# Kernel optimization log

Measured on AMD Instinct MI355X. Metric: run time of the kernel, lower is better.

Reference implementation:

```python
import jax, jax.numpy as jnp
import numpy as np

NEG_SLOPE = 0.01  # nn.LeakyReLU default

def _leaky(x):
    return jnp.where(x >= 0, x, NEG_SLOPE * x)

def setup_inputs() -> dict:
    key = jax.random.key(0)
    ks = jax.random.split(key, 8)
    in_ch = 64
    B, H, W = 8, 256, 256
    x = jax.random.normal(ks[0], (B, 2 * in_ch, H, W), dtype=jnp.float32)
    dims = [(64, 128), (32, 64), (16, 32), (8, 16), (4, 8), (2, 4), (1, 2)]
    inp = {"x": x}
    for i, (o, c) in enumerate(dims):
        # kaiming_normal_ fan_out, relu: std = sqrt(2 / fan_out), fan_out = o*1*1
        std = np.sqrt(2.0 / o).astype(np.float32)
        inp[f"w{i+1}"] = jax.random.normal(ks[i + 1], (o, c), dtype=jnp.float32) * std
    return inp

def reference(x, w1, w2, w3, w4, w5, w6, w7):
    # Each 1x1 conv (bias-free) is a per-pixel matmul over channels.
    h = x
    for w in (w1, w2, w3, w4, w5, w6):
        h = _leaky(jnp.einsum('bchw,oc->bohw', h, w))
    out = jnp.einsum('bchw,oc->bohw', h, w7)  # final conv, no activation
    return out
```

## Files before the change

kernel.cpp:

```cpp
#include <hip/hip_runtime.h>


#define NEG_SLOPE 0.01f

typedef __attribute__((ext_vector_type(8))) short bf16x8;
typedef __attribute__((ext_vector_type(4))) float f32x4;

__device__ __forceinline__ float leaky(float v) { return v >= 0.f ? v : NEG_SLOPE * v; }

__device__ __forceinline__ short f2b(float f) {
    unsigned u = __float_as_uint(f);
    u += 0x7fffu + ((u >> 16) & 1u);
    return (short)(u >> 16);
}

__device__ __forceinline__ unsigned pk(float a, float b) {
    return (unsigned)(unsigned short)f2b(a) | ((unsigned)(unsigned short)f2b(b) << 16);
}

__device__ __forceinline__ bf16x8 loadA(const float* __restrict__ wsrc, int C, int m, int k) {
    const float* pr = wsrc + m * C + k;
    f32x4 lo = *(const f32x4*)pr;
    f32x4 hi = *(const f32x4*)(pr + 4);
    bf16x8 r;
    r[0] = f2b(lo[0]); r[1] = f2b(lo[1]); r[2] = f2b(lo[2]); r[3] = f2b(lo[3]);
    r[4] = f2b(hi[0]); r[5] = f2b(hi[1]); r[6] = f2b(hi[2]); r[7] = f2b(hi[3]);
    return r;
}

__global__ __launch_bounds__(256) void fused_mfma_kernel(
    const float* __restrict__ x,
    const float* __restrict__ w1, const float* __restrict__ w2,
    const float* __restrict__ w3, const float* __restrict__ w4,
    const float* __restrict__ w5, const float* __restrict__ w6,
    const float* __restrict__ w7, float* __restrict__ out) {
    constexpr int HW = 65536;

    __shared__ short lds_h1[4][16 * 72];
    __shared__ short lds_h2[4][16 * 40];
    __shared__ float lds_h3[4][64 * 17];
    __shared__ float lds_tw[176];

    const int tid = threadIdx.x;
    if (tid < 128)      lds_tw[tid] = w4[tid];
    else if (tid < 160) lds_tw[tid] = w5[tid - 128];
    else if (tid < 168) lds_tw[tid] = w6[tid - 160];
    else if (tid < 170) lds_tw[tid] = w7[tid - 168];
    __syncthreads();

    const int w    = tid >> 6;
    const int lane = tid & 63;
    const int p    = lane & 15;
    const int q    = lane >> 4;

    const int px0   = blockIdx.x * 256 + w * 64;
    const int batch = px0 >> 16;
    const int pin   = px0 & (HW - 1);
    const float* xb = x + (size_t)batch * 128 * HW;

    bf16x8 a1[4][4];
#pragma unroll
    for (int Mt = 0; Mt < 4; ++Mt)
#pragma unroll
        for (int Ks = 0; Ks < 4; ++Ks)
            a1[Mt][Ks] = loadA(w1, 128, Mt * 16 + p, Ks * 32 + q * 8);
    bf16x8 a2[2][2];
#pragma unroll
    for (int Mt = 0; Mt < 2; ++Mt)
#pragma unroll
        for (int Ks = 0; Ks < 2; ++Ks)
            a2[Mt][Ks] = loadA(w2, 64, Mt * 16 + p, Ks * 32 + q * 8);
    bf16x8 a3 = loadA(w3, 32, p, q * 8);

#pragma unroll
    for (int Nt = 0; Nt < 4; ++Nt) {
        const float* xp = xb + pin + Nt * 16 + p;

        bf16x8 bx[4];
#pragma unroll
        for (int Ks = 0; Ks < 4; ++Ks) {
            float t[8];
#pragma unroll
            for (int j = 0; j < 8; ++j)
                t[j] = xp[(size_t)(Ks * 32 + q * 8 + j) * HW];
#pragma unroll
            for (int j = 0; j < 8; ++j) bx[Ks][j] = f2b(t[j]);
        }

        f32x4 d1[4];
#pragma unroll
        for (int Mt = 0; Mt < 4; ++Mt) {
            f32x4 acc = {0.f, 0.f, 0.f, 0.f};
#pragma unroll
            for (int Ks = 0; Ks < 4; ++Ks)
                acc = __builtin_amdgcn_mfma_f32_16x16x32_bf16(a1[Mt][Ks], bx[Ks], acc, 0, 0, 0);
            d1[Mt] = acc;
        }

        {
            short* h1w = &lds_h1[w][p * 72];
#pragma unroll
            for (int Mt = 0; Mt < 4; ++Mt) {
                uint2 v;
                v.x = pk(leaky(d1[Mt][0]), leaky(d1[Mt][1]));
                v.y = pk(leaky(d1[Mt][2]), leaky(d1[Mt][3]));
                *(uint2*)(h1w + Mt * 16 + q * 4) = v;
            }
        }

        bf16x8 b2[2];
#pragma unroll
        for (int Ks = 0; Ks < 2; ++Ks)
            b2[Ks] = *(const bf16x8*)&lds_h1[w][p * 72 + Ks * 32 + q * 8];

        f32x4 d2[2];
#pragma unroll
        for (int Mt = 0; Mt < 2; ++Mt) {
            f32x4 acc = {0.f, 0.f, 0.f, 0.f};
#pragma unroll
            for (int Ks = 0; Ks < 2; ++Ks)
                acc = __builtin_amdgcn_mfma_f32_16x16x32_bf16(a2[Mt][Ks], b2[Ks], acc, 0, 0, 0);
            d2[Mt] = acc;
        }

        {
            short* h2w = &lds_h2[w][p * 40];
#pragma unroll
            for (int Mt = 0; Mt < 2; ++Mt) {
                uint2 v;
                v.x = pk(leaky(d2[Mt][0]), leaky(d2[Mt][1]));
                v.y = pk(leaky(d2[Mt][2]), leaky(d2[Mt][3]));
                *(uint2*)(h2w + Mt * 16 + q * 4) = v;
            }
        }

        bf16x8 b3 = *(const bf16x8*)&lds_h2[w][p * 40 + q * 8];
        f32x4 zero = {0.f, 0.f, 0.f, 0.f};
        f32x4 d3 = __builtin_amdgcn_mfma_f32_16x16x32_bf16(a3, b3, zero, 0, 0, 0);

        {
            float* h3w = &lds_h3[w][(Nt * 16 + p) * 17 + q * 4];
            h3w[0] = leaky(d3[0]);
            h3w[1] = leaky(d3[1]);
            h3w[2] = leaky(d3[2]);
            h3w[3] = leaky(d3[3]);
        }
    }

    const float* h3r = &lds_h3[w][lane * 17];
    float h[16];
#pragma unroll
    for (int c = 0; c < 16; ++c) h[c] = h3r[c];

    float g4[8];
#pragma unroll
    for (int o = 0; o < 8; ++o) {
        float a = 0.f;
#pragma unroll
        for (int c = 0; c < 16; ++c) a = fmaf(lds_tw[o * 16 + c], h[c], a);
        g4[o] = leaky(a);
    }
    float g5[4];
#pragma unroll
    for (int o = 0; o < 4; ++o) {
        float a = 0.f;
#pragma unroll
        for (int c = 0; c < 8; ++c) a = fmaf(lds_tw[128 + o * 8 + c], g4[c], a);
        g5[o] = leaky(a);
    }
    float g6[2];
#pragma unroll
    for (int o = 0; o < 2; ++o) {
        float a = 0.f;
#pragma unroll
        for (int c = 0; c < 4; ++c) a = fmaf(lds_tw[160 + o * 4 + c], g5[c], a);
        g6[o] = leaky(a);
    }
    out[px0 + lane] = fmaf(lds_tw[168], g6[0], lds_tw[169] * g6[1]);
}

extern "C" void kernel_launch(void* const* d_in, const int* in_sizes, int n_in,
                              void* d_out, int out_size, void* d_ws, size_t ws_size,
                              hipStream_t stream) {
    const float* x  = (const float*)d_in[0];
    const float* w1 = (const float*)d_in[1];
    const float* w2 = (const float*)d_in[2];
    const float* w3 = (const float*)d_in[3];
    const float* w4 = (const float*)d_in[4];
    const float* w5 = (const float*)d_in[5];
    const float* w6 = (const float*)d_in[6];
    const float* w7 = (const float*)d_in[7];
    float* out = (float*)d_out;

    const int P = 8 * 256 * 256;
    fused_mfma_kernel<<<P / 256, 256, 0, stream>>>(x, w1, w2, w3, w4, w5, w6, w7, out);
}
```

Measured before the change: 439.7 us.

## Stage input channels through double-buffered LDS with async global-to-LDS copies

The kernel now loads x with 16-byte-per-lane async global_load_lds copies into a double-buffered LDS tile of 32 channels by 128 pixels. The first-layer MFMA loop iterates over K-chunks with the next chunk prefetched, replacing the old narrow, poorly coalesced per-lane scalar loads strided by HW. Blocks now cover 128 pixels (32 per wave, two N-tiles), and the intermediate LDS buffers are unioned into one per-wave scratch area. Occupancy is hinted via launch_bounds(256,2). The trade-off is extra block barriers per K-chunk and only half the lanes active in the scalar tail layers.

```diff
diff --git a/kernel.cpp b/kernel.cpp
--- a/kernel.cpp
+++ b/kernel.cpp
@@ -2,9 +2,11 @@
 
 
 #define NEG_SLOPE 0.01f
+constexpr int HW = 65536;
 
 typedef __attribute__((ext_vector_type(8))) short bf16x8;
 typedef __attribute__((ext_vector_type(4))) float f32x4;
+typedef __attribute__((ext_vector_type(2))) float f32x2;
 
 __device__ __forceinline__ float leaky(float v) { return v >= 0.f ? v : NEG_SLOPE * v; }
 
@@ -13,32 +15,33 @@
     u += 0x7fffu + ((u >> 16) & 1u);
     return (short)(u >> 16);
 }
-
-__device__ __forceinline__ unsigned pk(float a, float b) {
+__device__ __forceinline__ unsigned pk2(float a, float b) {
     return (unsigned)(unsigned short)f2b(a) | ((unsigned)(unsigned short)f2b(b) << 16);
 }
 
 __device__ __forceinline__ bf16x8 loadA(const float* __restrict__ wsrc, int C, int m, int k) {
-    const float* pr = wsrc + m * C + k;
-    f32x4 lo = *(const f32x4*)pr;
-    f32x4 hi = *(const f32x4*)(pr + 4);
-    bf16x8 r;
-    r[0] = f2b(lo[0]); r[1] = f2b(lo[1]); r[2] = f2b(lo[2]); r[3] = f2b(lo[3]);
-    r[4] = f2b(hi[0]); r[5] = f2b(hi[1]); r[6] = f2b(hi[2]); r[7] = f2b(hi[3]);
-    return r;
-}
-
-__global__ __launch_bounds__(256) void fused_mfma_kernel(
+    f32x4 lo = *(const f32x4*)(wsrc + m * C + k);
+    f32x4 hi = *(const f32x4*)(wsrc + m * C + k + 4);
+    union { bf16x8 v; unsigned u[4]; } r;
+    r.u[0] = pk2(lo[0], lo[1]); r.u[1] = pk2(lo[2], lo[3]);
+    r.u[2] = pk2(hi[0], hi[1]); r.u[3] = pk2(hi[2], hi[3]);
+    return r.v;
+}
+
+__device__ __forceinline__ void async_cp16(const float* g, float* l) {
+    __builtin_amdgcn_global_load_lds((const __attribute__((address_space(1))) unsigned*)g,
+                                     (__attribute__((address_space(3))) unsigned*)l,
+                                     16, 0, 0);
+}
+
+__global__ __launch_bounds__(256, 2) void fused_staged_kernel(
     const float* __restrict__ x,
     const float* __restrict__ w1, const float* __restrict__ w2,
     const float* __restrict__ w3, const float* __restrict__ w4,
     const float* __restrict__ w5, const float* __restrict__ w6,
     const float* __restrict__ w7, float* __restrict__ out) {
-    constexpr int HW = 65536;
-
-    __shared__ short lds_h1[4][16 * 72];
-    __shared__ short lds_h2[4][16 * 40];
-    __shared__ float lds_h3[4][64 * 17];
+    __shared__ float lds_x[2][32 * 128];
+    __shared__ unsigned long long lds_un[4][544];
     __shared__ float lds_tw[176];
 
     const int tid = threadIdx.x;
@@ -46,118 +49,150 @@
     else if (tid < 160) lds_tw[tid] = w5[tid - 128];
     else if (tid < 168) lds_tw[tid] = w6[tid - 160];
     else if (tid < 170) lds_tw[tid] = w7[tid - 168];
-    __syncthreads();
 
     const int w    = tid >> 6;
     const int lane = tid & 63;
-    const int p    = lane & 15;
+    const int n    = lane & 15;
     const int q    = lane >> 4;
-
-    const int px0   = blockIdx.x * 256 + w * 64;
+    const int half = lane >> 5;
+    const int pl   = lane & 31;
+
+    const int px0   = blockIdx.x * 128;
     const int batch = px0 >> 16;
     const int pin   = px0 & (HW - 1);
-    const float* xb = x + (size_t)batch * 128 * HW;
+    const float* xg = x + (size_t)batch * 128 * HW + pin;
+
+#pragma unroll
+    for (int i = 0; i < 4; ++i) {
+        int cp = w * 8 + 2 * i;
+        const float* g = xg + (size_t)(cp + half) * HW + pl * 4;
+        async_cp16(g, &lds_x[0][cp * 128]);
+    }
 
     bf16x8 a1[4][4];
 #pragma unroll
     for (int Mt = 0; Mt < 4; ++Mt)
 #pragma unroll
-        for (int Ks = 0; Ks < 4; ++Ks)
-            a1[Mt][Ks] = loadA(w1, 128, Mt * 16 + p, Ks * 32 + q * 8);
+        for (int kc = 0; kc < 4; ++kc)
+            a1[Mt][kc] = loadA(w1, 128, Mt * 16 + n, kc * 32 + q * 8);
     bf16x8 a2[2][2];
 #pragma unroll
     for (int Mt = 0; Mt < 2; ++Mt)
 #pragma unroll
-        for (int Ks = 0; Ks < 2; ++Ks)
-            a2[Mt][Ks] = loadA(w2, 64, Mt * 16 + p, Ks * 32 + q * 8);
-    bf16x8 a3 = loadA(w3, 32, p, q * 8);
-
-#pragma unroll
-    for (int Nt = 0; Nt < 4; ++Nt) {
-        const float* xp = xb + pin + Nt * 16 + p;
-
-        bf16x8 bx[4];
-#pragma unroll
-        for (int Ks = 0; Ks < 4; ++Ks) {
+        for (int kc = 0; kc < 2; ++kc)
+            a2[Mt][kc] = loadA(w2, 64, Mt * 16 + n, kc * 32 + q * 8);
+    bf16x8 a3 = loadA(w3, 32, n, q * 8);
+
+    __syncthreads();
+
+    f32x4 acc1[4][2];
+#pragma unroll
+    for (int Mt = 0; Mt < 4; ++Mt)
+#pragma unroll
+        for (int Nt = 0; Nt < 2; ++Nt) acc1[Mt][Nt] = (f32x4){0.f, 0.f, 0.f, 0.f};
+
+#pragma unroll
+    for (int kc = 0; kc < 4; ++kc) {
+        if (kc < 3) {
+#pragma unroll
+            for (int i = 0; i < 4; ++i) {
+                int cp = w * 8 + 2 * i;
+                const float* g = xg + (size_t)((kc + 1) * 32 + cp + half) * HW + pl * 4;
+                async_cp16(g, &lds_x[(kc + 1) & 1][cp * 128]);
+            }
+        }
+        const float* xb = &lds_x[kc & 1][0];
+#pragma unroll
+        for (int Nt = 0; Nt < 2; ++Nt) {
             float t[8];
 #pragma unroll
             for (int j = 0; j < 8; ++j)
-                t[j] = xp[(size_t)(Ks * 32 + q * 8 + j) * HW];
-#pragma unroll
-            for (int j = 0; j < 8; ++j) bx[Ks][j] = f2b(t[j]);
-        }
-
-        f32x4 d1[4];
-#pragma unroll
-        for (int Mt = 0; Mt < 4; ++Mt) {
-            f32x4 acc = {0.f, 0.f, 0.f, 0.f};
-#pragma unroll
-            for (int Ks = 0; Ks < 4; ++Ks)
-                acc = __builtin_amdgcn_mfma_f32_16x16x32_bf16(a1[Mt][Ks], bx[Ks], acc, 0, 0, 0);
-            d1[Mt] = acc;
-        }
-
-        {
-            short* h1w = &lds_h1[w][p * 72];
-#pragma unroll
-            for (int Mt = 0; Mt < 4; ++Mt) {
-                uint2 v;
-                v.x = pk(leaky(d1[Mt][0]), leaky(d1[Mt][1]));
-                v.y = pk(leaky(d1[Mt][2]), leaky(d1[Mt][3]));
-                *(uint2*)(h1w + Mt * 16 + q * 4) = v;
-            }
-        }
-
-        bf16x8 b2[2];
-#pragma unroll
-        for (int Ks = 0; Ks < 2; ++Ks)
-            b2[Ks] = *(const bf16x8*)&lds_h1[w][p * 72 + Ks * 32 + q * 8];
-
-        f32x4 d2[2];
-#pragma unroll
-        for (int Mt = 0; Mt < 2; ++Mt) {
-            f32x4 acc = {0.f, 0.f, 0.f, 0.f};
-#pragma unroll
-            for (int Ks = 0; Ks < 2; ++Ks)
-                acc = __builtin_amdgcn_mfma_f32_16x16x32_bf16(a2[Mt][Ks], b2[Ks], acc, 0, 0, 0);
-            d2[Mt] = acc;
-        }
-
-        {
-            short* h2w = &lds_h2[w][p * 40];
-#pragma unroll
-            for (int Mt = 0; Mt < 2; ++Mt) {
-                uint2 v;
-                v.x = pk(leaky(d2[Mt][0]), leaky(d2[Mt][1]));
-                v.y = pk(leaky(d2[Mt][2]), leaky(d2[Mt][3]));
-                *(uint2*)(h2w + Mt * 16 + q * 4) = v;
-            }
-        }
-
-        bf16x8 b3 = *(const bf16x8*)&lds_h2[w][p * 40 + q * 8];
+                t[j] = xb[(q * 8 + j) * 128 + w * 32 + Nt * 16 + n];
+            union { bf16x8 v; unsigned u[4]; } b;
+            b.u[0] = pk2(t[0], t[1]); b.u[1] = pk2(t[2], t[3]);
+            b.u[2] = pk2(t[4], t[5]); b.u[3] = pk2(t[6], t[7]);
+#pragma unroll
+            for (int Mt = 0; Mt < 4; ++Mt)
+                acc1[Mt][Nt] = __builtin_amdgcn_mfma_f32_16x16x32_bf16(a1[Mt][kc], b.v, acc1[Mt][Nt], 0, 0, 0);
+        }
+        if (kc < 3) __syncthreads();
+    }
+
+    short* h1 = (short*)&lds_un[w][0];
+#pragma unroll
+    for (int Mt = 0; Mt < 4; ++Mt)
+#pragma unroll
+        for (int Nt = 0; Nt < 2; ++Nt) {
+            int px = Nt * 16 + n;
+            uint2 v;
+            v.x = pk2(leaky(acc1[Mt][Nt][0]), leaky(acc1[Mt][Nt][1]));
+            v.y = pk2(leaky(acc1[Mt][Nt][2]), leaky(acc1[Mt][Nt][3]));
+            *(uint2*)(h1 + px * 68 + Mt * 16 + q * 4) = v;
+        }
+
+    f32x4 acc2[2][2];
+#pragma unroll
+    for (int Mt = 0; Mt < 2; ++Mt)
+#pragma unroll
+        for (int Nt = 0; Nt < 2; ++Nt) acc2[Mt][Nt] = (f32x4){0.f, 0.f, 0.f, 0.f};
+#pragma unroll
+    for (int Nt = 0; Nt < 2; ++Nt)
+#pragma unroll
+        for (int kc = 0; kc < 2; ++kc) {
+            int off = (Nt * 16 + n) * 68 + kc * 32 + q * 8;
+            uint2 lo = *(const uint2*)(h1 + off);
+            uint2 hi = *(const uint2*)(h1 + off + 4);
+            union { bf16x8 v; unsigned u[4]; } b;
+            b.u[0] = lo.x; b.u[1] = lo.y; b.u[2] = hi.x; b.u[3] = hi.y;
+#pragma unroll
+            for (int Mt = 0; Mt < 2; ++Mt)
+                acc2[Mt][Nt] = __builtin_amdgcn_mfma_f32_16x16x32_bf16(a2[Mt][kc], b.v, acc2[Mt][Nt], 0, 0, 0);
+        }
+
+    short* h2 = (short*)&lds_un[w][0];
+#pragma unroll
+    for (int Mt = 0; Mt < 2; ++Mt)
+#pragma unroll
+        for (int Nt = 0; Nt < 2; ++Nt) {
+            int px = Nt * 16 + n;
+            uint2 v;
+            v.x = pk2(leaky(acc2[Mt][Nt][0]), leaky(acc2[Mt][Nt][1]));
+            v.y = pk2(leaky(acc2[Mt][Nt][2]), leaky(acc2[Mt][Nt][3]));
+            *(uint2*)(h2 + px * 36 + Mt * 16 + q * 4) = v;
+        }
+
+    f32x4 acc3[2];
+#pragma unroll
+    for (int Nt = 0; Nt < 2; ++Nt) {
+        int off = (Nt * 16 + n) * 36 + q * 8;
+        uint2 lo = *(const uint2*)(h2 + off);
+        uint2 hi = *(const uint2*)(h2 + off + 4);
+        union { bf16x8 v; unsigned u[4]; } b;
+        b.u[0] = lo.x; b.u[1] = lo.y; b.u[2] = hi.x; b.u[3] = hi.y;
         f32x4 zero = {0.f, 0.f, 0.f, 0.f};
-        f32x4 d3 = __builtin_amdgcn_mfma_f32_16x16x32_bf16(a3, b3, zero, 0, 0, 0);
-
-        {
-            float* h3w = &lds_h3[w][(Nt * 16 + p) * 17 + q * 4];
-            h3w[0] = leaky(d3[0]);
-            h3w[1] = leaky(d3[1]);
-            h3w[2] = leaky(d3[2]);
-            h3w[3] = leaky(d3[3]);
-        }
-    }
-
-    const float* h3r = &lds_h3[w][lane * 17];
-    float h[16];
-#pragma unroll
-    for (int c = 0; c < 16; ++c) h[c] = h3r[c];
+        acc3[Nt] = __builtin_amdgcn_mfma_f32_16x16x32_bf16(a3, b.v, zero, 0, 0, 0);
+    }
+
+    float* h3 = (float*)&lds_un[w][0];
+#pragma unroll
+    for (int Nt = 0; Nt < 2; ++Nt) {
+        int px = Nt * 16 + n;
+        f32x2 va = {leaky(acc3[Nt][0]), leaky(acc3[Nt][1])};
+        f32x2 vb = {leaky(acc3[Nt][2]), leaky(acc3[Nt][3])};
+        *(f32x2*)(h3 + px * 18 + q * 4)     = va;
+        *(f32x2*)(h3 + px * 18 + q * 4 + 2) = vb;
+    }
+
+    float hh[16];
+#pragma unroll
+    for (int c = 0; c < 16; ++c) hh[c] = h3[pl * 18 + c];
 
     float g4[8];
 #pragma unroll
     for (int o = 0; o < 8; ++o) {
         float a = 0.f;
 #pragma unroll
-        for (int c = 0; c < 16; ++c) a = fmaf(lds_tw[o * 16 + c], h[c], a);
+        for (int c = 0; c < 16; ++c) a = fmaf(lds_tw[o * 16 + c], hh[c], a);
         g4[o] = leaky(a);
     }
     float g5[4];
@@ -176,7 +211,8 @@
         for (int c = 0; c < 4; ++c) a = fmaf(lds_tw[160 + o * 4 + c], g5[c], a);
         g6[o] = leaky(a);
     }
-    out[px0 + lane] = fmaf(lds_tw[168], g6[0], lds_tw[169] * g6[1]);
+    float res = fmaf(lds_tw[168], g6[0], lds_tw[169] * g6[1]);
+    if (lane < 32) out[px0 + w * 32 + pl] = res;
 }
 
 extern "C" void kernel_launch(void* const* d_in, const int* in_sizes, int n_in,
@@ -193,5 +229,5 @@
     float* out = (float*)d_out;
 
     const int P = 8 * 256 * 256;
-    fused_mfma_kernel<<<P / 256, 256, 0, stream>>>(x, w1, w2, w3, w4, w5, w6, w7, out);
-}
+    fused_staged_kernel<<<P / 128, 256, 0, stream>>>(x, w1, w2, w3, w4, w5, w6, w7, out);
+}
```

Result: faster. 402.7 us (-8.4%).
